# Kernel tuning notes

Hardware: AMD Instinct MI355X
Metric: run time of the kernel (lower is better)

The kernel has to match this reference:

```python
import jax, jax.numpy as jnp
import numpy as np

N_NODES = 1_000_000
N_EDGES = 32_000_000
DC = 16
HIDDEN = 32
EPS = 1e-8
LN_EPS = 1e-5


def _harmonic_encoding(x, dC):
    # x: [n] curvature in [-1,1]; returns [n, dC] (dC even here)
    norm = jnp.clip((x + 1.0) / (2.0 + EPS), 0.0, 1.0)
    freqs = jnp.arange(1, dC // 2 + 1, dtype=x.dtype) * jnp.pi  # [dC/2]
    ang = norm[:, None] * freqs[None, :]                        # [n, dC/2]
    # interleave sin/cos exactly like torch.stack(...,dim=2).view(n,dC)
    return jnp.stack([jnp.sin(ang), jnp.cos(ang)], axis=2).reshape(x.shape[0], dC)


def setup_inputs() -> dict:
    key = jax.random.key(0)
    k_orc, k_ei, k_w1, k_w2, k_g = jax.random.split(key, 5)
    node_orc = jax.random.uniform(k_orc, (N_NODES,), dtype=jnp.float32) * 2.0 - 1.0
    edge_index = jax.random.randint(k_ei, (2, N_EDGES), 0, N_NODES, dtype=jnp.int64)
    # MLP params (torch Linear convention: W [out, in])
    W1 = jax.random.normal(k_w1, (HIDDEN, DC), dtype=jnp.float32) * (1.0 / np.sqrt(DC))
    b1 = jnp.zeros((HIDDEN,), dtype=jnp.float32)
    W2 = jax.random.normal(k_w2, (DC, HIDDEN), dtype=jnp.float32) * (1.0 / np.sqrt(HIDDEN))
    b2 = jnp.zeros((DC,), dtype=jnp.float32)
    gamma = jnp.ones((DC,), dtype=jnp.float32)
    beta = jnp.zeros((DC,), dtype=jnp.float32)
    return {"node_orc": node_orc, "edge_index": edge_index,
            "W1": W1, "b1": b1, "W2": W2, "b2": b2,
            "gamma": gamma, "beta": beta}


def _neighbor_mean(node_orc, edge_index):
    src, dst = edge_index[0], edge_index[1]
    n = node_orc.shape[0]
    deg = jnp.zeros((n,), node_orc.dtype).at[src].add(1.0).at[dst].add(1.0)
    s = (jnp.zeros((n,), node_orc.dtype)
         .at[src].add(node_orc[dst])
         .at[dst].add(node_orc[src]))
    return jnp.where(deg > 0, s / jnp.where(deg > 0, deg, 1.0), 0.0)


def reference(node_orc, edge_index, W1, b1, W2, b2, gamma, beta):
    # advanced harmonic encoding: node encoding + neighbor-mean encoding
    nb_mean = _neighbor_mean(node_orc, edge_index)
    Phi_base = jnp.concatenate(
        [_harmonic_encoding(node_orc, DC // 2),
         _harmonic_encoding(nb_mean, DC // 2)], axis=1)      # [n, 16]
    # learnable MLP (dropout in eval = identity) + LayerNorm + residual
    h = jax.nn.relu(jnp.einsum('nd,hd->nh', Phi_base, W1) + b1)
    y = jnp.einsum('nh,dh->nd', h, W2) + b2
    mu = jnp.mean(y, axis=-1, keepdims=True)
    var = jnp.var(y, axis=-1, keepdims=True)
    y = (y - mu) / jnp.sqrt(var + LN_EPS) * gamma + beta
    return y + Phi_base
```

## Files before the change

kernel.cpp:

```cpp
#include <hip/hip_runtime.h>

constexpr int kNodes = 1000000;
constexpr int kEdges = 32000000;

constexpr int NB = 256;
constexpr int BSHIFT = 12;
constexpr int BNODES = 4096;
constexpr int NBUSED = (kNodes + BNODES - 1) / BNODES;
constexpr int EPT = 4096;
constexpr int TILES = (kEdges + EPT - 1) / EPT;
constexpr int SLOT = 72;
constexpr int GP = SLOT / 4;
constexpr int CAP = 284672;
constexpr int SPLIT = 2;
constexpr unsigned PADREC = 0x10000000u;
constexpr unsigned OVFCAP = 8192;

constexpr size_t kArenaBytes = (size_t)NBUSED * CAP * 4;
constexpr size_t kCurOff    = kArenaBytes;
constexpr size_t kCurBytes  = (size_t)NB * 64 + 64;
constexpr size_t kAccOff    = kCurOff + kCurBytes;
constexpr size_t kAccBytes  = (size_t)SPLIT * kNodes * 4;
constexpr size_t kOrcqOff   = kAccOff + kAccBytes;
constexpr size_t kOrcqBytes = (size_t)kNodes * 2;
constexpr size_t kOvfOff    = (kOrcqOff + kOrcqBytes + 7) & ~(size_t)7;
constexpr size_t kOvfBytes  = (size_t)OVFCAP * 8;
constexpr size_t kWsNeeded  = kOvfOff + kOvfBytes;

__global__ __launch_bounds__(256) void quant_orc(
        const float* __restrict__ orc, unsigned short* __restrict__ orcq,
        unsigned* __restrict__ gcur) {
    if (blockIdx.x == 0) {
        if (threadIdx.x < NB) gcur[threadIdx.x * 16] = 0u;
        if (threadIdx.x == 0) gcur[NB * 16] = 0u;
    }
    const int i = (blockIdx.x * 256 + threadIdx.x) * 4;
    if (i >= kNodes) return;
    const float4 v = *reinterpret_cast<const float4*>(orc + i);
    unsigned q0 = __float2uint_rn((v.x + 1.0f) * 32768.0f);
    unsigned q1 = __float2uint_rn((v.y + 1.0f) * 32768.0f);
    unsigned q2 = __float2uint_rn((v.z + 1.0f) * 32768.0f);
    unsigned q3 = __float2uint_rn((v.w + 1.0f) * 32768.0f);
    q0 = q0 > 65535u ? 65535u : q0;
    q1 = q1 > 65535u ? 65535u : q1;
    q2 = q2 > 65535u ? 65535u : q2;
    q3 = q3 > 65535u ? 65535u : q3;
    ushort4 q;
    q.x = (unsigned short)q0; q.y = (unsigned short)q1;
    q.z = (unsigned short)q2; q.w = (unsigned short)q3;
    *reinterpret_cast<ushort4*>(orcq + i) = q;
}

__global__ __launch_bounds__(1024) void scatter_sort(
        const int* __restrict__ ei, const unsigned short* __restrict__ orcq,
        unsigned* __restrict__ arena, unsigned* __restrict__ gcur,
        unsigned long long* __restrict__ ovf) {
    __shared__ alignas(16) unsigned slab[NB * SLOT];
    __shared__ unsigned cnt[NB];
    __shared__ unsigned pcs[NB];
    __shared__ unsigned dstadd[NB];
    const int tid = threadIdx.x;
    const int t = blockIdx.x;
    const int e0 = t * EPT;
    const int ne = min(EPT, kEdges - e0);
    const int k4 = tid * 4;

    if (tid < NB) cnt[tid] = 0u;
    __syncthreads();

    if (k4 < ne) {
        const int4 s4 = *reinterpret_cast<const int4*>(ei + e0 + k4);
        const int4 d4 = *reinterpret_cast<const int4*>(ei + kEdges + e0 + k4);
        const unsigned a0 = orcq[d4.x], a1 = orcq[d4.y],
                       a2 = orcq[d4.z], a3 = orcq[d4.w];
        const unsigned b0 = orcq[s4.x], b1 = orcq[s4.y],
                       b2 = orcq[s4.z], b3 = orcq[s4.w];
        #define RANK1(N, Q) { \
            const unsigned b_ = (unsigned)(N) >> BSHIFT; \
            const unsigned r_ = atomicAdd(&cnt[b_], 1u); \
            if (r_ < (unsigned)SLOT) { \
                slab[b_ * SLOT + r_] = (((unsigned)(N) & (BNODES - 1)) << 16) | (Q); \
            } else { \
                const unsigned oi_ = atomicAdd(&gcur[NB * 16], 1u); \
                if (oi_ < OVFCAP) \
                    ovf[oi_] = ((unsigned long long)(unsigned)(N) << 16) | (Q); \
            } }
        RANK1(s4.x, a0) RANK1(s4.y, a1) RANK1(s4.z, a2) RANK1(s4.w, a3)
        RANK1(d4.x, b0) RANK1(d4.y, b1) RANK1(d4.z, b2) RANK1(d4.w, b3)
        #undef RANK1
    }
    __syncthreads();

    if (tid < NB) {
        unsigned c = cnt[tid];
        c = c > (unsigned)SLOT ? (unsigned)SLOT : c;
        const unsigned pc = (c + 3u) & ~3u;
        pcs[tid] = pc;
        unsigned g = atomicAdd(&gcur[tid * 16], pc);
        if (g + pc > (unsigned)CAP) g = CAP - pc;
        dstadd[tid] = (unsigned)tid * CAP + g;
        for (unsigned j = c; j < pc; ++j) slab[tid * SLOT + j] = PADREC;
    }
    __syncthreads();

    for (int k = tid; k < NB * GP; k += 1024) {
        const int b = k / GP;
        const int g4 = (k - b * GP) * 4;
        if ((unsigned)g4 < pcs[b]) {
            *reinterpret_cast<int4*>(arena + dstadd[b] + g4) =
                *reinterpret_cast<const int4*>(slab + b * SLOT + g4);
        }
    }
}

__global__ __launch_bounds__(1024) void bucket_accum(
        const unsigned* __restrict__ arena, const unsigned* __restrict__ gcur,
        unsigned* __restrict__ acc) {
    __shared__ unsigned lacc[2][BNODES + 4];
    const int tid = threadIdx.x;
    const int b = blockIdx.x >> 1;
    const int half = blockIdx.x & 1;
    for (int k = tid; k < 2 * (BNODES + 4); k += 1024)
        lacc[0][k] = 0u;
    __syncthreads();
    unsigned* __restrict__ my = lacc[(tid >> 6) & 1];
    unsigned len = gcur[b * 16];
    len = len > (unsigned)CAP ? (unsigned)CAP : len;
    const unsigned h = (len >> 1) & ~3u;
    const unsigned lo4 = (half ? h : 0u) >> 2;
    const unsigned hi4 = (half ? len : h) >> 2;
    const uint4* __restrict__ p =
        reinterpret_cast<const uint4*>(arena + (size_t)b * CAP);
    for (unsigned i = lo4 + tid; i < hi4; i += 1024) {
        const uint4 v = p[i];
        atomicAdd(&my[v.x >> 16], (v.x & 0xFFFFu) | 0x1000000u);
        atomicAdd(&my[v.y >> 16], (v.y & 0xFFFFu) | 0x1000000u);
        atomicAdd(&my[v.z >> 16], (v.z & 0xFFFFu) | 0x1000000u);
        atomicAdd(&my[v.w >> 16], (v.w & 0xFFFFu) | 0x1000000u);
    }
    __syncthreads();
    const int base = b << BSHIFT;
    unsigned* __restrict__ dst = acc + (size_t)half * kNodes;
    for (int k = tid; k < BNODES; k += 1024) {
        const int nn = base + k;
        if (nn < kNodes) dst[nn] = lacc[0][k] + lacc[1][k];
    }
}

__global__ __launch_bounds__(256) void ovf_fix(
        const unsigned long long* __restrict__ ovf,
        const unsigned* __restrict__ gcur, unsigned* __restrict__ acc) {
    unsigned n = gcur[NB * 16];
    n = n > OVFCAP ? OVFCAP : n;
    for (unsigned i = threadIdx.x; i < n; i += 256) {
        const unsigned long long v = ovf[i];
        atomicAdd(&acc[(unsigned)(v >> 16)],
                  ((unsigned)v & 0xFFFFu) | 0x1000000u);
    }
}

constexpr float kScale = 1048576.0f;
constexpr float kInvScale = 1.0f / 1048576.0f;
constexpr long long kBias = 1ll << 36;

__global__ __launch_bounds__(256) void zero_acc(unsigned long long* __restrict__ acc) {
    int i = blockIdx.x * 256 + threadIdx.x;
    if (i < kNodes) acc[i] = 0ull;
}

__global__ __launch_bounds__(256) void edge_kernel(
        const int* __restrict__ ei,
        const float* __restrict__ orc,
        unsigned long long* __restrict__ acc) {
    int t = blockIdx.x * 256 + threadIdx.x;
    int e0 = t * 4;
    if (e0 >= kEdges) return;
    const int4 s4 = *reinterpret_cast<const int4*>(ei + e0);
    const int4 d4 = *reinterpret_cast<const int4*>(ei + kEdges + e0);
    const int ss[4] = {s4.x, s4.y, s4.z, s4.w};
    const int dd[4] = {d4.x, d4.y, d4.z, d4.w};
    #pragma unroll
    for (int k = 0; k < 4; ++k) {
        const float os = orc[ss[k]];
        const float od = orc[dd[k]];
        const unsigned long long ps =
            (1ull << 48) + (unsigned long long)(kBias + (long long)__float2ll_rn(od * kScale));
        const unsigned long long pd =
            (1ull << 48) + (unsigned long long)(kBias + (long long)__float2ll_rn(os * kScale));
        atomicAdd(&acc[ss[k]], ps);
        atomicAdd(&acc[dd[k]], pd);
    }
}

template <int MODE>
__global__ __launch_bounds__(256) void node_kernel(
        const float* __restrict__ orc,
        const unsigned long long* __restrict__ acc64,
        const unsigned* __restrict__ acc32,
        const float* __restrict__ W1, const float* __restrict__ b1,
        const float* __restrict__ W2, const float* __restrict__ b2,
        const float* __restrict__ gamma, const float* __restrict__ beta,
        float* __restrict__ out) {
    const int i = blockIdx.x * 256 + threadIdx.x;
    if (i >= kNodes) return;

    const float x0 = orc[i];
    float nb;
    if (MODE == 0) {
        const unsigned long long p = acc64[i];
        const unsigned deg = (unsigned)(p >> 48);
        const long long sf = (long long)(p & ((1ull << 48) - 1)) - (long long)deg * kBias;
        const float s = (float)sf * kInvScale;
        nb = (deg > 0) ? s / (float)deg : 0.0f;
    } else {
        const unsigned p0 = acc32[i];
        const unsigned p1 = acc32[kNodes + i];
        const unsigned deg = (p0 >> 24) + (p1 >> 24);
        const unsigned sumq = (p0 & 0xFFFFFFu) + (p1 & 0xFFFFFFu);
        nb = (deg > 0)
            ? ((float)sumq * (1.0f / 32768.0f) / (float)deg - 1.0f) : 0.0f;
    }

    constexpr float kPi = 3.14159265358979323846f;
    float Phi[16];
    const float n0 = __saturatef((x0 + 1.0f) * 0.5f);
    const float n1 = __saturatef((nb + 1.0f) * 0.5f);
    #pragma unroll
    for (int k = 0; k < 4; ++k) {
        const float a0 = n0 * (float)(k + 1) * kPi;
        const float a1 = n1 * (float)(k + 1) * kPi;
        Phi[2 * k]     = __sinf(a0);
        Phi[2 * k + 1] = __cosf(a0);
        Phi[8 + 2 * k]     = __sinf(a1);
        Phi[8 + 2 * k + 1] = __cosf(a1);
    }

    float y[16];
    #pragma unroll
    for (int d = 0; d < 16; ++d) y[d] = b2[d];
    #pragma unroll
    for (int j = 0; j < 32; ++j) {
        float a = b1[j];
        #pragma unroll
        for (int d = 0; d < 16; ++d) a = fmaf(Phi[d], W1[j * 16 + d], a);
        a = fmaxf(a, 0.0f);
        #pragma unroll
        for (int d = 0; d < 16; ++d) y[d] = fmaf(a, W2[d * 32 + j], y[d]);
    }

    float mu = 0.0f;
    #pragma unroll
    for (int d = 0; d < 16; ++d) mu += y[d];
    mu *= (1.0f / 16.0f);
    float var = 0.0f;
    #pragma unroll
    for (int d = 0; d < 16; ++d) { const float t = y[d] - mu; var = fmaf(t, t, var); }
    var *= (1.0f / 16.0f);
    const float inv = rsqrtf(var + 1e-5f);

    float4* o4 = reinterpret_cast<float4*>(out + (size_t)i * 16);
    #pragma unroll
    for (int q = 0; q < 4; ++q) {
        float4 o;
        o.x = (y[4 * q + 0] - mu) * inv * gamma[4 * q + 0] + beta[4 * q + 0] + Phi[4 * q + 0];
        o.y = (y[4 * q + 1] - mu) * inv * gamma[4 * q + 1] + beta[4 * q + 1] + Phi[4 * q + 1];
        o.z = (y[4 * q + 2] - mu) * inv * gamma[4 * q + 2] + beta[4 * q + 2] + Phi[4 * q + 2];
        o.w = (y[4 * q + 3] - mu) * inv * gamma[4 * q + 3] + beta[4 * q + 3] + Phi[4 * q + 3];
        o4[q] = o;
    }
}

extern "C" void kernel_launch(void* const* d_in, const int* in_sizes, int n_in,
                              void* d_out, int out_size, void* d_ws, size_t ws_size,
                              hipStream_t stream) {
    const float* orc   = (const float*)d_in[0];
    const int*   ei    = (const int*)d_in[1];
    const float* W1    = (const float*)d_in[2];
    const float* b1    = (const float*)d_in[3];
    const float* W2    = (const float*)d_in[4];
    const float* b2    = (const float*)d_in[5];
    const float* gamma = (const float*)d_in[6];
    const float* beta  = (const float*)d_in[7];
    float* out = (float*)d_out;
    char* ws = (char*)d_ws;

    if (ws_size >= kWsNeeded) {
        unsigned* arena = (unsigned*)ws;
        unsigned* gcur = (unsigned*)(ws + kCurOff);
        unsigned* acc = (unsigned*)(ws + kAccOff);
        unsigned short* orcq = (unsigned short*)(ws + kOrcqOff);
        unsigned long long* ovf = (unsigned long long*)(ws + kOvfOff);
        quant_orc<<<(kNodes / 4 + 255) / 256, 256, 0, stream>>>(orc, orcq, gcur);
        scatter_sort<<<TILES, 1024, 0, stream>>>(ei, orcq, arena, gcur, ovf);
        bucket_accum<<<NBUSED * SPLIT, 1024, 0, stream>>>(arena, gcur, acc);
        ovf_fix<<<1, 256, 0, stream>>>(ovf, gcur, acc);
        node_kernel<3><<<(kNodes + 255) / 256, 256, 0, stream>>>(
            orc, nullptr, acc, W1, b1, W2, b2, gamma, beta, out);
    } else {
        unsigned long long* acc = (unsigned long long*)ws;
        zero_acc<<<(kNodes + 255) / 256, 256, 0, stream>>>(acc);
        edge_kernel<<<(kEdges / 4 + 255) / 256, 256, 0, stream>>>(ei, orc, acc);
        node_kernel<0><<<(kNodes + 255) / 256, 256, 0, stream>>>(
            orc, acc, nullptr, W1, b1, W2, b2, gamma, beta, out);
    }
}
```

Measured before the change: 708.9 us.

## Process two edge tiles per scatter block with early gathers and unroll accumulation

Each scatter_sort block now handles two edge tiles. It issues both tiles' index loads and orcq gathers up front, before the shared-memory ranking passes, so global latency overlaps with the atomic and flush phases. SLOT shrinks from 72 to 64 so slab indexing becomes shifts, and launch bounds are raised. bucket_accum's loop is unrolled by two to put more loads in flight. The smaller slot is expected to send more records to the overflow path, which is capped at OVFCAP and could drop records or add global atomics.

```diff
diff --git a/kernel.cpp b/kernel.cpp
--- a/kernel.cpp
+++ b/kernel.cpp
@@ -9,7 +9,7 @@
 constexpr int NBUSED = (kNodes + BNODES - 1) / BNODES;
 constexpr int EPT = 4096;
 constexpr int TILES = (kEdges + EPT - 1) / EPT;
-constexpr int SLOT = 72;
+constexpr int SLOT = 64;
 constexpr int GP = SLOT / 4;
 constexpr int CAP = 284672;
 constexpr int SPLIT = 2;
@@ -51,77 +51,117 @@
     *reinterpret_cast<ushort4*>(orcq + i) = q;
 }
 
-__global__ __launch_bounds__(1024) void scatter_sort(
+__global__ __launch_bounds__(1024, 8) void scatter_sort(
         const int* __restrict__ ei, const unsigned short* __restrict__ orcq,
         unsigned* __restrict__ arena, unsigned* __restrict__ gcur,
         unsigned long long* __restrict__ ovf) {
     __shared__ alignas(16) unsigned slab[NB * SLOT];
-    __shared__ unsigned cnt[NB];
+    __shared__ unsigned cntA[NB], cntB[NB];
     __shared__ unsigned pcs[NB];
     __shared__ unsigned dstadd[NB];
     const int tid = threadIdx.x;
-    const int t = blockIdx.x;
-    const int e0 = t * EPT;
-    const int ne = min(EPT, kEdges - e0);
+    const int tA = blockIdx.x * 2;
+    const int tB = tA + 1;
     const int k4 = tid * 4;
 
-    if (tid < NB) cnt[tid] = 0u;
-    __syncthreads();
-
-    if (k4 < ne) {
-        const int4 s4 = *reinterpret_cast<const int4*>(ei + e0 + k4);
-        const int4 d4 = *reinterpret_cast<const int4*>(ei + kEdges + e0 + k4);
-        const unsigned a0 = orcq[d4.x], a1 = orcq[d4.y],
-                       a2 = orcq[d4.z], a3 = orcq[d4.w];
-        const unsigned b0 = orcq[s4.x], b1 = orcq[s4.y],
-                       b2 = orcq[s4.z], b3 = orcq[s4.w];
-        #define RANK1(N, Q) { \
-            const unsigned b_ = (unsigned)(N) >> BSHIFT; \
-            const unsigned r_ = atomicAdd(&cnt[b_], 1u); \
-            if (r_ < (unsigned)SLOT) { \
-                slab[b_ * SLOT + r_] = (((unsigned)(N) & (BNODES - 1)) << 16) | (Q); \
-            } else { \
-                const unsigned oi_ = atomicAdd(&gcur[NB * 16], 1u); \
-                if (oi_ < OVFCAP) \
-                    ovf[oi_] = ((unsigned long long)(unsigned)(N) << 16) | (Q); \
-            } }
-        RANK1(s4.x, a0) RANK1(s4.y, a1) RANK1(s4.z, a2) RANK1(s4.w, a3)
-        RANK1(d4.x, b0) RANK1(d4.y, b1) RANK1(d4.z, b2) RANK1(d4.w, b3)
-        #undef RANK1
-    }
-    __syncthreads();
-
-    if (tid < NB) {
-        unsigned c = cnt[tid];
-        c = c > (unsigned)SLOT ? (unsigned)SLOT : c;
-        const unsigned pc = (c + 3u) & ~3u;
-        pcs[tid] = pc;
-        unsigned g = atomicAdd(&gcur[tid * 16], pc);
-        if (g + pc > (unsigned)CAP) g = CAP - pc;
-        dstadd[tid] = (unsigned)tid * CAP + g;
-        for (unsigned j = c; j < pc; ++j) slab[tid * SLOT + j] = PADREC;
-    }
-    __syncthreads();
-
-    for (int k = tid; k < NB * GP; k += 1024) {
-        const int b = k / GP;
-        const int g4 = (k - b * GP) * 4;
-        if ((unsigned)g4 < pcs[b]) {
-            *reinterpret_cast<int4*>(arena + dstadd[b] + g4) =
-                *reinterpret_cast<const int4*>(slab + b * SLOT + g4);
-        }
-    }
+    const int neA = min(EPT, kEdges - tA * EPT);
+    const bool actA = k4 < neA;
+    int4 sA, dA; sA.x = sA.y = sA.z = sA.w = 0; dA = sA;
+    unsigned pA0 = 0, pA1 = 0, pA2 = 0, pA3 = 0;
+    if (actA) {
+        sA = *reinterpret_cast<const int4*>(ei + tA * EPT + k4);
+        dA = *reinterpret_cast<const int4*>(ei + kEdges + tA * EPT + k4);
+        const unsigned a0 = orcq[dA.x], a1 = orcq[dA.y],
+                       a2 = orcq[dA.z], a3 = orcq[dA.w];
+        const unsigned b0 = orcq[sA.x], b1 = orcq[sA.y],
+                       b2 = orcq[sA.z], b3 = orcq[sA.w];
+        pA0 = a0 | (b0 << 16); pA1 = a1 | (b1 << 16);
+        pA2 = a2 | (b2 << 16); pA3 = a3 | (b3 << 16);
+    }
+    const int neB = (tB < TILES) ? min(EPT, kEdges - tB * EPT) : 0;
+    const bool actB = k4 < neB;
+    int4 sB, dB; sB.x = sB.y = sB.z = sB.w = 0; dB = sB;
+    unsigned pB0 = 0, pB1 = 0, pB2 = 0, pB3 = 0;
+    if (actB) {
+        sB = *reinterpret_cast<const int4*>(ei + tB * EPT + k4);
+        dB = *reinterpret_cast<const int4*>(ei + kEdges + tB * EPT + k4);
+        const unsigned a0 = orcq[dB.x], a1 = orcq[dB.y],
+                       a2 = orcq[dB.z], a3 = orcq[dB.w];
+        const unsigned b0 = orcq[sB.x], b1 = orcq[sB.y],
+                       b2 = orcq[sB.z], b3 = orcq[sB.w];
+        pB0 = a0 | (b0 << 16); pB1 = a1 | (b1 << 16);
+        pB2 = a2 | (b2 << 16); pB3 = a3 | (b3 << 16);
+    }
+
+    if (tid < NB) { cntA[tid] = 0u; cntB[tid] = 0u; }
+    __syncthreads();
+
+    #define RANK1(CNT, N, Q) { \
+        const unsigned b_ = (unsigned)(N) >> BSHIFT; \
+        const unsigned r_ = atomicAdd(&CNT[b_], 1u); \
+        if (r_ < (unsigned)SLOT) { \
+            slab[(b_ << 6) + r_] = (((unsigned)(N) & (BNODES - 1)) << 16) | (Q); \
+        } else { \
+            const unsigned oi_ = atomicAdd(&gcur[NB * 16], 1u); \
+            if (oi_ < OVFCAP) \
+                ovf[oi_] = ((unsigned long long)(unsigned)(N) << 16) | (Q); \
+        } }
+
+    #define ALLOC(CNT) { \
+        unsigned c_ = CNT[tid]; \
+        c_ = c_ > (unsigned)SLOT ? (unsigned)SLOT : c_; \
+        const unsigned pc_ = (c_ + 3u) & ~3u; \
+        pcs[tid] = pc_; \
+        unsigned g_ = atomicAdd(&gcur[tid * 16], pc_); \
+        if (g_ + pc_ > (unsigned)CAP) g_ = CAP - pc_; \
+        dstadd[tid] = (unsigned)tid * CAP + g_; \
+        for (unsigned j_ = c_; j_ < pc_; ++j_) slab[(tid << 6) + j_] = PADREC; }
+
+    #define FLUSH { \
+        for (int k_ = tid; k_ < NB * GP; k_ += 1024) { \
+            const int b_ = k_ >> 4; \
+            const int g4_ = (k_ & 15) << 2; \
+            if ((unsigned)g4_ < pcs[b_]) \
+                *reinterpret_cast<int4*>(arena + dstadd[b_] + g4_) = \
+                    *reinterpret_cast<const int4*>(slab + (b_ << 6) + g4_); \
+        } }
+
+    if (actA) {
+        RANK1(cntA, sA.x, pA0 & 0xFFFFu) RANK1(cntA, sA.y, pA1 & 0xFFFFu)
+        RANK1(cntA, sA.z, pA2 & 0xFFFFu) RANK1(cntA, sA.w, pA3 & 0xFFFFu)
+        RANK1(cntA, dA.x, pA0 >> 16)     RANK1(cntA, dA.y, pA1 >> 16)
+        RANK1(cntA, dA.z, pA2 >> 16)     RANK1(cntA, dA.w, pA3 >> 16)
+    }
+    __syncthreads();
+    if (tid < NB) ALLOC(cntA)
+    __syncthreads();
+    FLUSH
+    __syncthreads();
+    if (actB) {
+        RANK1(cntB, sB.x, pB0 & 0xFFFFu) RANK1(cntB, sB.y, pB1 & 0xFFFFu)
+        RANK1(cntB, sB.z, pB2 & 0xFFFFu) RANK1(cntB, sB.w, pB3 & 0xFFFFu)
+        RANK1(cntB, dB.x, pB0 >> 16)     RANK1(cntB, dB.y, pB1 >> 16)
+        RANK1(cntB, dB.z, pB2 >> 16)     RANK1(cntB, dB.w, pB3 >> 16)
+    }
+    __syncthreads();
+    if (tid < NB) ALLOC(cntB)
+    __syncthreads();
+    FLUSH
+
+    #undef RANK1
+    #undef ALLOC
+    #undef FLUSH
 }
 
 __global__ __launch_bounds__(1024) void bucket_accum(
         const unsigned* __restrict__ arena, const unsigned* __restrict__ gcur,
         unsigned* __restrict__ acc) {
     __shared__ unsigned lacc[2][BNODES + 4];
+    unsigned* __restrict__ flat = &lacc[0][0];
     const int tid = threadIdx.x;
     const int b = blockIdx.x >> 1;
     const int half = blockIdx.x & 1;
-    for (int k = tid; k < 2 * (BNODES + 4); k += 1024)
-        lacc[0][k] = 0u;
+    for (int k = tid; k < 2 * (BNODES + 4); k += 1024) flat[k] = 0u;
     __syncthreads();
     unsigned* __restrict__ my = lacc[(tid >> 6) & 1];
     unsigned len = gcur[b * 16];
@@ -131,7 +171,20 @@
     const unsigned hi4 = (half ? len : h) >> 2;
     const uint4* __restrict__ p =
         reinterpret_cast<const uint4*>(arena + (size_t)b * CAP);
-    for (unsigned i = lo4 + tid; i < hi4; i += 1024) {
+    unsigned i = lo4 + tid;
+    for (; i + 1024 < hi4; i += 2048) {
+        const uint4 v0 = p[i];
+        const uint4 v1 = p[i + 1024];
+        atomicAdd(&my[v0.x >> 16], (v0.x & 0xFFFFu) | 0x1000000u);
+        atomicAdd(&my[v0.y >> 16], (v0.y & 0xFFFFu) | 0x1000000u);
+        atomicAdd(&my[v0.z >> 16], (v0.z & 0xFFFFu) | 0x1000000u);
+        atomicAdd(&my[v0.w >> 16], (v0.w & 0xFFFFu) | 0x1000000u);
+        atomicAdd(&my[v1.x >> 16], (v1.x & 0xFFFFu) | 0x1000000u);
+        atomicAdd(&my[v1.y >> 16], (v1.y & 0xFFFFu) | 0x1000000u);
+        atomicAdd(&my[v1.z >> 16], (v1.z & 0xFFFFu) | 0x1000000u);
+        atomicAdd(&my[v1.w >> 16], (v1.w & 0xFFFFu) | 0x1000000u);
+    }
+    if (i < hi4) {
         const uint4 v = p[i];
         atomicAdd(&my[v.x >> 16], (v.x & 0xFFFFu) | 0x1000000u);
         atomicAdd(&my[v.y >> 16], (v.y & 0xFFFFu) | 0x1000000u);
@@ -291,7 +344,7 @@
         unsigned short* orcq = (unsigned short*)(ws + kOrcqOff);
         unsigned long long* ovf = (unsigned long long*)(ws + kOvfOff);
         quant_orc<<<(kNodes / 4 + 255) / 256, 256, 0, stream>>>(orc, orcq, gcur);
-        scatter_sort<<<TILES, 1024, 0, stream>>>(ei, orcq, arena, gcur, ovf);
+        scatter_sort<<<(TILES + 1) / 2, 1024, 0, stream>>>(ei, orcq, arena, gcur, ovf);
         bucket_accum<<<NBUSED * SPLIT, 1024, 0, stream>>>(arena, gcur, acc);
         ovf_fix<<<1, 256, 0, stream>>>(ovf, gcur, acc);
         node_kernel<3><<<(kNodes + 255) / 256, 256, 0, stream>>>(
```

Result: slower. 819.2 us (+15.6%).

## Defer neighbor value gather from scatter pass to bucket accumulation

Applied to the files above, without the earlier changes.

The scatter pass now stores the raw 20-bit neighbor index in each record instead of looking up its quantized curvature, so the random orcq gathers leave the edge-streaming kernel. The bucket accumulation kernel then gathers from a 1M-entry 4-byte table that already carries the degree increment, and handles two uint4 loads per iteration. It also drops the duplicated shared accumulator. The padding record now points to a zeroed table entry. The random gathers move to a later kernel and get wider (4 bytes instead of 2), and dropping the dual-LDS copy may raise atomic contention.

```diff
diff --git a/kernel.cpp b/kernel.cpp
--- a/kernel.cpp
+++ b/kernel.cpp
@@ -13,48 +13,50 @@
 constexpr int GP = SLOT / 4;
 constexpr int CAP = 284672;
 constexpr int SPLIT = 2;
-constexpr unsigned PADREC = 0x10000000u;
+constexpr unsigned PADREC = 0xFFFFFFFFu;
 constexpr unsigned OVFCAP = 8192;
+constexpr int QTABN = 1 << 20;
 
 constexpr size_t kArenaBytes = (size_t)NBUSED * CAP * 4;
 constexpr size_t kCurOff    = kArenaBytes;
 constexpr size_t kCurBytes  = (size_t)NB * 64 + 64;
 constexpr size_t kAccOff    = kCurOff + kCurBytes;
 constexpr size_t kAccBytes  = (size_t)SPLIT * kNodes * 4;
-constexpr size_t kOrcqOff   = kAccOff + kAccBytes;
-constexpr size_t kOrcqBytes = (size_t)kNodes * 2;
-constexpr size_t kOvfOff    = (kOrcqOff + kOrcqBytes + 7) & ~(size_t)7;
+constexpr size_t kQtabOff   = kAccOff + kAccBytes;
+constexpr size_t kQtabBytes = (size_t)QTABN * 4;
+constexpr size_t kOvfOff    = kQtabOff + kQtabBytes;
 constexpr size_t kOvfBytes  = (size_t)OVFCAP * 8;
 constexpr size_t kWsNeeded  = kOvfOff + kOvfBytes;
 
-__global__ __launch_bounds__(256) void quant_orc(
-        const float* __restrict__ orc, unsigned short* __restrict__ orcq,
+__global__ __launch_bounds__(256) void qtab_build(
+        const float* __restrict__ orc, unsigned* __restrict__ qtab,
         unsigned* __restrict__ gcur) {
     if (blockIdx.x == 0) {
         if (threadIdx.x < NB) gcur[threadIdx.x * 16] = 0u;
         if (threadIdx.x == 0) gcur[NB * 16] = 0u;
     }
     const int i = (blockIdx.x * 256 + threadIdx.x) * 4;
-    if (i >= kNodes) return;
-    const float4 v = *reinterpret_cast<const float4*>(orc + i);
-    unsigned q0 = __float2uint_rn((v.x + 1.0f) * 32768.0f);
-    unsigned q1 = __float2uint_rn((v.y + 1.0f) * 32768.0f);
-    unsigned q2 = __float2uint_rn((v.z + 1.0f) * 32768.0f);
-    unsigned q3 = __float2uint_rn((v.w + 1.0f) * 32768.0f);
-    q0 = q0 > 65535u ? 65535u : q0;
-    q1 = q1 > 65535u ? 65535u : q1;
-    q2 = q2 > 65535u ? 65535u : q2;
-    q3 = q3 > 65535u ? 65535u : q3;
-    ushort4 q;
-    q.x = (unsigned short)q0; q.y = (unsigned short)q1;
-    q.z = (unsigned short)q2; q.w = (unsigned short)q3;
-    *reinterpret_cast<ushort4*>(orcq + i) = q;
+    if (i < kNodes) {
+        const float4 v = *reinterpret_cast<const float4*>(orc + i);
+        unsigned q0 = __float2uint_rn((v.x + 1.0f) * 32768.0f);
+        unsigned q1 = __float2uint_rn((v.y + 1.0f) * 32768.0f);
+        unsigned q2 = __float2uint_rn((v.z + 1.0f) * 32768.0f);
+        unsigned q3 = __float2uint_rn((v.w + 1.0f) * 32768.0f);
+        uint4 q;
+        q.x = (q0 > 65535u ? 65535u : q0) | 0x1000000u;
+        q.y = (q1 > 65535u ? 65535u : q1) | 0x1000000u;
+        q.z = (q2 > 65535u ? 65535u : q2) | 0x1000000u;
+        q.w = (q3 > 65535u ? 65535u : q3) | 0x1000000u;
+        *reinterpret_cast<uint4*>(qtab + i) = q;
+    } else if (i < QTABN) {
+        uint4 z; z.x = z.y = z.z = z.w = 0u;
+        *reinterpret_cast<uint4*>(qtab + i) = z;
+    }
 }
 
 __global__ __launch_bounds__(1024) void scatter_sort(
-        const int* __restrict__ ei, const unsigned short* __restrict__ orcq,
-        unsigned* __restrict__ arena, unsigned* __restrict__ gcur,
-        unsigned long long* __restrict__ ovf) {
+        const int* __restrict__ ei, unsigned* __restrict__ arena,
+        unsigned* __restrict__ gcur, unsigned long long* __restrict__ ovf) {
     __shared__ alignas(16) unsigned slab[NB * SLOT];
     __shared__ unsigned cnt[NB];
     __shared__ unsigned pcs[NB];
@@ -71,22 +73,20 @@
     if (k4 < ne) {
         const int4 s4 = *reinterpret_cast<const int4*>(ei + e0 + k4);
         const int4 d4 = *reinterpret_cast<const int4*>(ei + kEdges + e0 + k4);
-        const unsigned a0 = orcq[d4.x], a1 = orcq[d4.y],
-                       a2 = orcq[d4.z], a3 = orcq[d4.w];
-        const unsigned b0 = orcq[s4.x], b1 = orcq[s4.y],
-                       b2 = orcq[s4.z], b3 = orcq[s4.w];
-        #define RANK1(N, Q) { \
+        #define RANK1(N, O) { \
             const unsigned b_ = (unsigned)(N) >> BSHIFT; \
             const unsigned r_ = atomicAdd(&cnt[b_], 1u); \
             if (r_ < (unsigned)SLOT) { \
-                slab[b_ * SLOT + r_] = (((unsigned)(N) & (BNODES - 1)) << 16) | (Q); \
+                slab[b_ * SLOT + r_] = \
+                    (((unsigned)(N) & (BNODES - 1)) << 20) | (unsigned)(O); \
             } else { \
                 const unsigned oi_ = atomicAdd(&gcur[NB * 16], 1u); \
                 if (oi_ < OVFCAP) \
-                    ovf[oi_] = ((unsigned long long)(unsigned)(N) << 16) | (Q); \
+                    ovf[oi_] = ((unsigned long long)(unsigned)(N) << 32) | \
+                               (unsigned)(O); \
             } }
-        RANK1(s4.x, a0) RANK1(s4.y, a1) RANK1(s4.z, a2) RANK1(s4.w, a3)
-        RANK1(d4.x, b0) RANK1(d4.y, b1) RANK1(d4.z, b2) RANK1(d4.w, b3)
+        RANK1(s4.x, d4.x) RANK1(s4.y, d4.y) RANK1(s4.z, d4.z) RANK1(s4.w, d4.w)
+        RANK1(d4.x, s4.x) RANK1(d4.y, s4.y) RANK1(d4.z, s4.z) RANK1(d4.w, s4.w)
         #undef RANK1
     }
     __syncthreads();
@@ -115,15 +115,13 @@
 
 __global__ __launch_bounds__(1024) void bucket_accum(
         const unsigned* __restrict__ arena, const unsigned* __restrict__ gcur,
-        unsigned* __restrict__ acc) {
-    __shared__ unsigned lacc[2][BNODES + 4];
+        const unsigned* __restrict__ qtab, unsigned* __restrict__ acc) {
+    __shared__ unsigned lacc[BNODES];
     const int tid = threadIdx.x;
     const int b = blockIdx.x >> 1;
     const int half = blockIdx.x & 1;
-    for (int k = tid; k < 2 * (BNODES + 4); k += 1024)
-        lacc[0][k] = 0u;
-    __syncthreads();
-    unsigned* __restrict__ my = lacc[(tid >> 6) & 1];
+    for (int k = tid; k < BNODES; k += 1024) lacc[k] = 0u;
+    __syncthreads();
     unsigned len = gcur[b * 16];
     len = len > (unsigned)CAP ? (unsigned)CAP : len;
     const unsigned h = (len >> 1) & ~3u;
@@ -131,31 +129,52 @@
     const unsigned hi4 = (half ? len : h) >> 2;
     const uint4* __restrict__ p =
         reinterpret_cast<const uint4*>(arena + (size_t)b * CAP);
-    for (unsigned i = lo4 + tid; i < hi4; i += 1024) {
+    unsigned i = lo4 + tid;
+    for (; i + 1024 < hi4; i += 2048) {
+        const uint4 v0 = p[i];
+        const uint4 v1 = p[i + 1024];
+        const unsigned q0 = qtab[v0.x & 0xFFFFFu];
+        const unsigned q1 = qtab[v0.y & 0xFFFFFu];
+        const unsigned q2 = qtab[v0.z & 0xFFFFFu];
+        const unsigned q3 = qtab[v0.w & 0xFFFFFu];
+        const unsigned q4 = qtab[v1.x & 0xFFFFFu];
+        const unsigned q5 = qtab[v1.y & 0xFFFFFu];
+        const unsigned q6 = qtab[v1.z & 0xFFFFFu];
+        const unsigned q7 = qtab[v1.w & 0xFFFFFu];
+        atomicAdd(&lacc[v0.x >> 20], q0);
+        atomicAdd(&lacc[v0.y >> 20], q1);
+        atomicAdd(&lacc[v0.z >> 20], q2);
+        atomicAdd(&lacc[v0.w >> 20], q3);
+        atomicAdd(&lacc[v1.x >> 20], q4);
+        atomicAdd(&lacc[v1.y >> 20], q5);
+        atomicAdd(&lacc[v1.z >> 20], q6);
+        atomicAdd(&lacc[v1.w >> 20], q7);
+    }
+    if (i < hi4) {
         const uint4 v = p[i];
-        atomicAdd(&my[v.x >> 16], (v.x & 0xFFFFu) | 0x1000000u);
-        atomicAdd(&my[v.y >> 16], (v.y & 0xFFFFu) | 0x1000000u);
-        atomicAdd(&my[v.z >> 16], (v.z & 0xFFFFu) | 0x1000000u);
-        atomicAdd(&my[v.w >> 16], (v.w & 0xFFFFu) | 0x1000000u);
+        atomicAdd(&lacc[v.x >> 20], qtab[v.x & 0xFFFFFu]);
+        atomicAdd(&lacc[v.y >> 20], qtab[v.y & 0xFFFFFu]);
+        atomicAdd(&lacc[v.z >> 20], qtab[v.z & 0xFFFFFu]);
+        atomicAdd(&lacc[v.w >> 20], qtab[v.w & 0xFFFFFu]);
     }
     __syncthreads();
     const int base = b << BSHIFT;
     unsigned* __restrict__ dst = acc + (size_t)half * kNodes;
     for (int k = tid; k < BNODES; k += 1024) {
         const int nn = base + k;
-        if (nn < kNodes) dst[nn] = lacc[0][k] + lacc[1][k];
+        if (nn < kNodes) dst[nn] = lacc[k];
     }
 }
 
 __global__ __launch_bounds__(256) void ovf_fix(
         const unsigned long long* __restrict__ ovf,
-        const unsigned* __restrict__ gcur, unsigned* __restrict__ acc) {
+        const unsigned* __restrict__ gcur, const unsigned* __restrict__ qtab,
+        unsigned* __restrict__ acc) {
     unsigned n = gcur[NB * 16];
     n = n > OVFCAP ? OVFCAP : n;
     for (unsigned i = threadIdx.x; i < n; i += 256) {
         const unsigned long long v = ovf[i];
-        atomicAdd(&acc[(unsigned)(v >> 16)],
-                  ((unsigned)v & 0xFFFFu) | 0x1000000u);
+        atomicAdd(&acc[(unsigned)(v >> 32)], qtab[(unsigned)v & 0xFFFFFu]);
     }
 }
 
@@ -288,12 +307,12 @@
         unsigned* arena = (unsigned*)ws;
         unsigned* gcur = (unsigned*)(ws + kCurOff);
         unsigned* acc = (unsigned*)(ws + kAccOff);
-        unsigned short* orcq = (unsigned short*)(ws + kOrcqOff);
+        unsigned* qtab = (unsigned*)(ws + kQtabOff);
         unsigned long long* ovf = (unsigned long long*)(ws + kOvfOff);
-        quant_orc<<<(kNodes / 4 + 255) / 256, 256, 0, stream>>>(orc, orcq, gcur);
-        scatter_sort<<<TILES, 1024, 0, stream>>>(ei, orcq, arena, gcur, ovf);
-        bucket_accum<<<NBUSED * SPLIT, 1024, 0, stream>>>(arena, gcur, acc);
-        ovf_fix<<<1, 256, 0, stream>>>(ovf, gcur, acc);
+        qtab_build<<<QTABN / 4 / 256, 256, 0, stream>>>(orc, qtab, gcur);
+        scatter_sort<<<TILES, 1024, 0, stream>>>(ei, arena, gcur, ovf);
+        bucket_accum<<<NBUSED * SPLIT, 1024, 0, stream>>>(arena, gcur, qtab, acc);
+        ovf_fix<<<1, 256, 0, stream>>>(ovf, gcur, qtab, acc);
         node_kernel<3><<<(kNodes + 255) / 256, 256, 0, stream>>>(
             orc, nullptr, acc, W1, b1, W2, b2, gamma, beta, out);
     } else {
```

After: 894.4 us. 1.26x slower.
